# Kernel optimization log

Measured on AMD Instinct MI355X. Metric: run time of the kernel, lower is better.

The kernel has to match this reference:

```python
import jax, jax.numpy as jnp
import numpy as np

N_FFT = 100
CROP = int(np.ceil(N_FFT / 2))  # 50, non-redundant frequency components
D = 2 * CROP                    # MVN dimensionality
LOG_2PI = float(np.log(2.0 * np.pi))


def setup_inputs() -> dict:
    key = jax.random.key(0)
    B = 262144
    x = jax.random.normal(key, (B, N_FFT), dtype=jnp.float32)
    return {"x": x}


def reference(x):
    # Batched, vectorized equivalent of the per-sample numpy FFT loop:
    # fftshift(fft(x))[:CROP] / N_FFT, split into real/imag channels.
    X = jnp.fft.fftshift(jnp.fft.fft(x, axis=-1), axes=-1)[:, :CROP]  # [B, CROP] complex64
    x_fft = jnp.stack([jnp.real(X), jnp.imag(X)], axis=1) / N_FFT     # [B, 2, CROP] float32
    # Standard-normal MVN log-prob (zero mean, identity cov) over flattened [B, D].
    z = x_fft.reshape(x_fft.shape[0], -1)
    log_pz = -0.5 * jnp.sum(z * z, axis=-1) - 0.5 * D * LOG_2PI       # [B]
    # log_jacob is the constant 0 in the original module; omitted as non-tensor.
    return (x_fft, log_pz)
```

## Files before the change

kernel.cpp:

```cpp
#include <hip/hip_runtime.h>
#include <math.h>


#define NFFT 100
#define CROP 50
#define BLOCK 256
#define TM 64
#define STRIDE 108
#define LOGPZ_CONST -91.893853320467274f

__device__ float g_W[NFFT * NFFT];

__global__ void init_w_kernel() {
    int idx = blockIdx.x * blockDim.x + threadIdx.x;
    if (idx < NFFT * NFFT) {
        int j = idx / NFFT;
        int n = idx - j * NFFT;
        int bin = (j < CROP) ? (CROP + j) : j;
        int t = (bin * n) % NFFT;
        float ang = (float)t * 0.06283185307179586477f;
        g_W[idx] = ((j < CROP) ? cosf(ang) : -sinf(ang)) * 0.01f;
    }
}

__global__ __launch_bounds__(BLOCK) void dft_kernel(const float* __restrict__ x,
                                                    float* __restrict__ out,
                                                    int B) {
    __shared__ float tile[TM][STRIDE];
    __shared__ float p2[4][TM];

    const int tid  = threadIdx.x;
    const int lane = tid & 63;
    const int wv   = __builtin_amdgcn_readfirstlane(tid >> 6);
    const int blockBase = blockIdx.x * TM;

    const float* __restrict__ src = x + (size_t)blockBase * NFFT;
#pragma unroll
    for (int i = 0; i < 25; ++i) {
        int e  = tid + i * BLOCK;
        int rr = e / NFFT;
        int cc = e - rr * NFFT;
        tile[rr][cc] = src[e];
    }
    __syncthreads();

    const float* __restrict__ Wb = g_W + wv * 25 * NFFT;
    float acc[25];
#pragma unroll
    for (int j = 0; j < 25; ++j) acc[j] = 0.0f;

    const float4* __restrict__ xrow =
        reinterpret_cast<const float4*>(&tile[lane][0]);

    for (int kc = 0; kc < 25; ++kc) {
        float4 xv = xrow[kc];
#pragma unroll
        for (int j = 0; j < 25; ++j) {
            const float* wr = Wb + j * NFFT + kc * 4;
            acc[j] = fmaf(xv.x, wr[0], acc[j]);
            acc[j] = fmaf(xv.y, wr[1], acc[j]);
            acc[j] = fmaf(xv.z, wr[2], acc[j]);
            acc[j] = fmaf(xv.w, wr[3], acc[j]);
        }
    }

    float s2 = 0.0f;
#pragma unroll
    for (int j = 0; j < 25; ++j) s2 = fmaf(acc[j], acc[j], s2);
    p2[wv][lane] = s2;

    __syncthreads();

#pragma unroll
    for (int j = 0; j < 25; ++j) tile[lane][wv * 25 + j] = acc[j];
    __syncthreads();

    float* __restrict__ dst = out + (size_t)blockBase * NFFT;
#pragma unroll
    for (int i = 0; i < 25; ++i) {
        int e  = tid + i * BLOCK;
        int rr = e / NFFT;
        int cc = e - rr * NFFT;
        dst[e] = tile[rr][cc];
    }

    if (wv == 0) {
        float t = p2[0][lane] + p2[1][lane] + p2[2][lane] + p2[3][lane];
        out[(size_t)B * NFFT + blockBase + lane] = fmaf(t, -0.5f, LOGPZ_CONST);
    }
}

extern "C" void kernel_launch(void* const* d_in, const int* in_sizes, int n_in,
                              void* d_out, int out_size, void* d_ws, size_t ws_size,
                              hipStream_t stream) {
    const float* x = (const float*)d_in[0];
    float* out = (float*)d_out;
    const int B = in_sizes[0] / NFFT;

    hipLaunchKernelGGL(init_w_kernel, dim3((NFFT * NFFT + BLOCK - 1) / BLOCK),
                       dim3(BLOCK), 0, stream);
    hipLaunchKernelGGL(dft_kernel, dim3(B / TM), dim3(BLOCK), 0, stream, x, out, B);
}
```

Baseline: 237.7 us.

## Exploit real-input DFT symmetry with even/odd folding and cache twiddles in LDS

Folds each input row into even (x[n]+x[N-n]) and odd (x[n]-x[N-n]) halves so the cosine outputs use only the even part and the sine outputs only the odd part. This roughly halves the FMA count per output. The twiddle matrix is shrunk to 100x52, staged into shared memory per block and read as float4 instead of as scalar global loads. The cost is a larger LDS footprint per block (about 48KB), which may reduce occupancy, plus a per-block twiddle copy.

```diff
diff --git a/kernel.cpp b/kernel.cpp
--- a/kernel.cpp
+++ b/kernel.cpp
@@ -2,65 +2,78 @@
 #include <math.h>
 
 
-#define NFFT 100
-#define CROP 50
+#define NFFT  100
+#define CROP  50
 #define BLOCK 256
-#define TM 64
-#define STRIDE 108
+#define TM    64
+#define EOS   108
+#define OSTR  101
+#define WROW  52
 #define LOGPZ_CONST -91.893853320467274f
 
-__device__ float g_W[NFFT * NFFT];
+__device__ float g_W2[NFFT * WROW];
 
 __global__ void init_w_kernel() {
     int idx = blockIdx.x * blockDim.x + threadIdx.x;
-    if (idx < NFFT * NFFT) {
-        int j = idx / NFFT;
-        int n = idx - j * NFFT;
+    if (idx < NFFT * WROW) {
+        int j = idx / WROW;
+        int n = idx - j * WROW;
         int bin = (j < CROP) ? (CROP + j) : j;
         int t = (bin * n) % NFFT;
         float ang = (float)t * 0.06283185307179586477f;
-        g_W[idx] = ((j < CROP) ? cosf(ang) : -sinf(ang)) * 0.01f;
+        float v = 0.0f;
+        if (j < CROP) {
+            if (n <= 50) v = cosf(ang) * 0.01f;
+        } else {
+            if (n >= 1 && n <= 49) v = -sinf(ang) * 0.01f;
+        }
+        g_W2[idx] = v;
     }
 }
 
 __global__ __launch_bounds__(BLOCK) void dft_kernel(const float* __restrict__ x,
                                                     float* __restrict__ out,
                                                     int B) {
-    __shared__ float tile[TM][STRIDE];
+    __shared__ float eo[TM * EOS];
+    __shared__ float wlds[NFFT * WROW];
     __shared__ float p2[4][TM];
 
     const int tid  = threadIdx.x;
     const int lane = tid & 63;
-    const int wv   = __builtin_amdgcn_readfirstlane(tid >> 6);
-    const int blockBase = blockIdx.x * TM;
+    const int wv   = tid >> 6;
+    const size_t base = (size_t)blockIdx.x * TM * NFFT;
+    const float* __restrict__ src = x + base;
 
-    const float* __restrict__ src = x + (size_t)blockBase * NFFT;
+    for (int i = tid; i < NFFT * WROW; i += BLOCK) wlds[i] = g_W2[i];
+
 #pragma unroll
-    for (int i = 0; i < 25; ++i) {
-        int e  = tid + i * BLOCK;
-        int rr = e / NFFT;
-        int cc = e - rr * NFFT;
-        tile[rr][cc] = src[e];
+    for (int i = 0; i < 13; ++i) {
+        int e2 = tid + i * BLOCK;
+        int rr = e2 / WROW;
+        int cc = e2 - rr * WROW;
+        float v1 = (cc <= 50) ? src[rr * NFFT + cc] : 0.0f;
+        float v2 = (cc >= 1 && cc <= 49) ? src[rr * NFFT + NFFT - cc] : 0.0f;
+        eo[rr * EOS + cc]        = v1 + v2;
+        eo[rr * EOS + WROW + cc] = v1 - v2;
     }
     __syncthreads();
 
-    const float* __restrict__ Wb = g_W + wv * 25 * NFFT;
+    const float* __restrict__ wbase = wlds + wv * 25 * WROW;
+    const float* __restrict__ xrow  = eo + lane * EOS + ((wv >= 2) ? WROW : 0);
+
     float acc[25];
 #pragma unroll
     for (int j = 0; j < 25; ++j) acc[j] = 0.0f;
 
-    const float4* __restrict__ xrow =
-        reinterpret_cast<const float4*>(&tile[lane][0]);
-
-    for (int kc = 0; kc < 25; ++kc) {
-        float4 xv = xrow[kc];
+    for (int kc = 0; kc < 13; ++kc) {
+        float4 xv = *reinterpret_cast<const float4*>(xrow + kc * 4);
 #pragma unroll
         for (int j = 0; j < 25; ++j) {
-            const float* wr = Wb + j * NFFT + kc * 4;
-            acc[j] = fmaf(xv.x, wr[0], acc[j]);
-            acc[j] = fmaf(xv.y, wr[1], acc[j]);
-            acc[j] = fmaf(xv.z, wr[2], acc[j]);
-            acc[j] = fmaf(xv.w, wr[3], acc[j]);
+            float4 w4 = *reinterpret_cast<const float4*>(wbase + j * WROW + kc * 4);
+            acc[j] = fmaf(xv.x, w4.x, acc[j]);
+            acc[j] = fmaf(xv.y, w4.y, acc[j]);
+            acc[j] = fmaf(xv.z, w4.z, acc[j]);
+            acc[j] = fmaf(xv.w, w4.w, acc[j]);
         }
     }
 
@@ -72,21 +85,21 @@
     __syncthreads();
 
 #pragma unroll
-    for (int j = 0; j < 25; ++j) tile[lane][wv * 25 + j] = acc[j];
+    for (int j = 0; j < 25; ++j) eo[lane * OSTR + wv * 25 + j] = acc[j];
     __syncthreads();
 
-    float* __restrict__ dst = out + (size_t)blockBase * NFFT;
+    float* __restrict__ dst = out + base;
 #pragma unroll
     for (int i = 0; i < 25; ++i) {
         int e  = tid + i * BLOCK;
         int rr = e / NFFT;
         int cc = e - rr * NFFT;
-        dst[e] = tile[rr][cc];
+        dst[e] = eo[rr * OSTR + cc];
     }
 
     if (wv == 0) {
         float t = p2[0][lane] + p2[1][lane] + p2[2][lane] + p2[3][lane];
-        out[(size_t)B * NFFT + blockBase + lane] = fmaf(t, -0.5f, LOGPZ_CONST);
+        out[(size_t)B * NFFT + blockIdx.x * TM + lane] = fmaf(t, -0.5f, LOGPZ_CONST);
     }
 }
 
@@ -97,7 +110,7 @@
     float* out = (float*)d_out;
     const int B = in_sizes[0] / NFFT;
 
-    hipLaunchKernelGGL(init_w_kernel, dim3((NFFT * NFFT + BLOCK - 1) / BLOCK),
+    hipLaunchKernelGGL(init_w_kernel, dim3((NFFT * WROW + BLOCK - 1) / BLOCK),
                        dim3(BLOCK), 0, stream);
     hipLaunchKernelGGL(dft_kernel, dim3(B / TM), dim3(BLOCK), 0, stream, x, out, B);
 }
```

Result: slower. 261.9 us (+10.2%).
